# Optimization experiments

Measured on AMD Instinct MI355X. Metric: run time of the kernel, lower is better.

## Reference

```python
import jax, jax.numpy as jnp
import numpy as np

D_MODEL, D_K, D_V, D_H, SEQ = 1024, 64, 64, 16, 4096


def setup_inputs() -> dict:
    key = jax.random.key(0)
    ks = jax.random.split(key, 16)
    s = lambda fan_in: 1.0 / np.sqrt(fan_in)
    return {
        "X": jax.random.normal(ks[0], (SEQ, D_MODEL), jnp.float32),
        # shared Q/K/V projections (nn.Linear stores weight as [out, in])
        "Wq": jax.random.uniform(ks[1], (D_K, D_MODEL), jnp.float32, -s(D_MODEL), s(D_MODEL)),
        "bq": jax.random.uniform(ks[2], (D_K,), jnp.float32, -s(D_MODEL), s(D_MODEL)),
        "Wk": jax.random.uniform(ks[3], (D_K, D_MODEL), jnp.float32, -s(D_MODEL), s(D_MODEL)),
        "bk": jax.random.uniform(ks[4], (D_K,), jnp.float32, -s(D_MODEL), s(D_MODEL)),
        "Wv": jax.random.uniform(ks[5], (D_V, D_MODEL), jnp.float32, -s(D_MODEL), s(D_MODEL)),
        "bv": jax.random.uniform(ks[6], (D_V,), jnp.float32, -s(D_MODEL), s(D_MODEL)),
        # per-head linears stacked along head axis
        "Whq": jax.random.uniform(ks[7], (D_H, D_K, D_K), jnp.float32, -s(D_K), s(D_K)),
        "bhq": jax.random.uniform(ks[8], (D_H, D_K), jnp.float32, -s(D_K), s(D_K)),
        "Whk": jax.random.uniform(ks[9], (D_H, D_K, D_K), jnp.float32, -s(D_K), s(D_K)),
        "bhk": jax.random.uniform(ks[10], (D_H, D_K), jnp.float32, -s(D_K), s(D_K)),
        "Whv": jax.random.uniform(ks[11], (D_H, D_V, D_V), jnp.float32, -s(D_V), s(D_V)),
        "bhv": jax.random.uniform(ks[12], (D_H, D_V), jnp.float32, -s(D_V), s(D_V)),
        # final projection: d_h*d_v -> d_model
        "Wo": jax.random.uniform(ks[13], (D_MODEL, D_H * D_V), jnp.float32, -s(D_H * D_V), s(D_H * D_V)),
        "bo": jax.random.uniform(ks[14], (D_MODEL,), jnp.float32, -s(D_H * D_V), s(D_H * D_V)),
    }


def reference(X, Wq, bq, Wk, bk, Wv, bv, Whq, bhq, Whk, bhk, Whv, bhv, Wo, bo):
    # shared projections: [T, d_k] / [T, d_v]
    Q = X @ Wq.T + bq
    K = X @ Wk.T + bk
    V = X @ Wv.T + bv
    # per-head linears, all heads at once: [H, T, d_k]
    qh = jnp.einsum("tk,hjk->htj", Q, Whq) + bhq[:, None, :]
    kh = jnp.einsum("tk,hjk->htj", K, Whk) + bhk[:, None, :]
    vh = jnp.einsum("tv,hjv->htj", V, Whv) + bhv[:, None, :]
    # scaled dot-product attention per head: [H, T, T]
    scale = 1.0 / jnp.sqrt(jnp.asarray(Q.shape[-1], X.dtype))
    attn = jax.nn.softmax(jnp.einsum("htk,hsk->hts", qh, kh) * scale, axis=-1)
    rep = jnp.einsum("hts,hsv->htv", attn, vh)  # [H, T, d_v]
    # hstack heads -> [T, H*d_v], then final projection
    concat = rep.transpose(1, 0, 2).reshape(X.shape[0], -1)
    return concat @ Wo.T + bo
```

## Files before the change

### kernel.cpp

```cpp
#include <hip/hip_runtime.h>

#define T 4096
#define DM 1024
#define DK 64
#define H 16

typedef short s8 __attribute__((ext_vector_type(8)));
typedef float f4 __attribute__((ext_vector_type(4)));
typedef unsigned short us4 __attribute__((ext_vector_type(4)));
typedef unsigned u32x4 __attribute__((ext_vector_type(4)));
typedef __bf16 bf2 __attribute__((ext_vector_type(2)));

#define MFMA16(a,b,c) __builtin_amdgcn_mfma_f32_16x16x32_bf16((a),(b),(c),0,0,0)
#define SCALE_Q 0.18033688011112042f

__device__ __forceinline__ unsigned short f2bf(float x){
  __bf16 b = (__bf16)x;
  return __builtin_bit_cast(unsigned short, b);
}
__device__ __forceinline__ unsigned pk2(float a, float b){
  bf2 v; v[0] = (__bf16)a; v[1] = (__bf16)b;
  return __builtin_bit_cast(unsigned, v);
}

__device__ __forceinline__ void gload16(const void* g, void* lds){
  __builtin_amdgcn_global_load_lds((const __attribute__((address_space(1))) unsigned int*)g,
                                   (__attribute__((address_space(3))) unsigned int*)lds,
                                   16, 0, 0);
}

__device__ __forceinline__ void xch(unsigned X, unsigned Y, unsigned &E, unsigned &O){
#if __has_builtin(__builtin_amdgcn_permlane32_swap) && __has_builtin(__builtin_amdgcn_permlane16_swap)
  auto a = __builtin_amdgcn_permlane32_swap(X, Y, false, false);
  auto b = __builtin_amdgcn_permlane16_swap(a[0], a[1], false, false);
  E = b[0]; O = b[1];
#else
  int l = threadIdx.x & 63;
  int idxE = ((((l >> 4) & 1) * 32 + (l & 15))) << 2;
  unsigned eX = __builtin_amdgcn_ds_bpermute(idxE, X);
  unsigned eY = __builtin_amdgcn_ds_bpermute(idxE, Y);
  E = (l < 32) ? eX : eY;
  unsigned oX = __builtin_amdgcn_ds_bpermute(idxE + 64, X);
  unsigned oY = __builtin_amdgcn_ds_bpermute(idxE + 64, Y);
  O = (l < 32) ? oX : oY;
#endif
}

__global__ void cvt_bf16(const float* __restrict__ in, unsigned short* __restrict__ out, int n4){
  int i = blockIdx.x * blockDim.x + threadIdx.x;
  if (i >= n4) return;
  float4 v = reinterpret_cast<const float4*>(in)[i];
  us4 o;
  o[0] = f2bf(v.x); o[1] = f2bf(v.y); o[2] = f2bf(v.z); o[3] = f2bf(v.w);
  reinterpret_cast<us4*>(out)[i] = o;
}

#define N_WOB (DM * DM / 4)
#define N_W3  (64 * DM / 4)
#define N_WH  (16 * 64 * 64 / 4)
__global__ __launch_bounds__(256) void prep_all(
    const float* __restrict__ Wo,
    const float* __restrict__ Wq, const float* __restrict__ Wk, const float* __restrict__ Wv,
    const float* __restrict__ Whq, const float* __restrict__ Whk, const float* __restrict__ Whv,
    const float* __restrict__ bq, const float* __restrict__ bk, const float* __restrict__ bv,
    const float* __restrict__ bhq, const float* __restrict__ bhk, const float* __restrict__ bhv,
    unsigned short* __restrict__ Wob, unsigned short* __restrict__ W3b,
    unsigned short* __restrict__ Whb, float* __restrict__ beff){
  int idx = blockIdx.x * 256 + threadIdx.x;
  if (idx < N_WOB){
    float4 v = reinterpret_cast<const float4*>(Wo)[idx];
    us4 o; o[0]=f2bf(v.x); o[1]=f2bf(v.y); o[2]=f2bf(v.z); o[3]=f2bf(v.w);
    reinterpret_cast<us4*>(Wob)[idx] = o;
    return;
  }
  idx -= N_WOB;
  if (idx < 3 * N_W3){
    int seg = idx / N_W3, i = idx - seg * N_W3;
    const float* src = (seg == 0) ? Wq : ((seg == 1) ? Wk : Wv);
    float4 v = reinterpret_cast<const float4*>(src)[i];
    us4 o; o[0]=f2bf(v.x); o[1]=f2bf(v.y); o[2]=f2bf(v.z); o[3]=f2bf(v.w);
    reinterpret_cast<us4*>(W3b)[seg * N_W3 + i] = o;
    return;
  }
  idx -= 3 * N_W3;
  if (idx < 3 * N_WH){
    int seg = idx / N_WH, i = idx - seg * N_WH;
    const float* src = (seg == 0) ? Whq : ((seg == 1) ? Whk : Whv);
    float s = (seg == 0) ? SCALE_Q : 1.0f;
    float4 v = reinterpret_cast<const float4*>(src)[i];
    us4 o; o[0]=f2bf(v.x*s); o[1]=f2bf(v.y*s); o[2]=f2bf(v.z*s); o[3]=f2bf(v.w*s);
    reinterpret_cast<us4*>(Whb)[seg * N_WH + i] = o;
    return;
  }
  idx -= 3 * N_WH;
  if (idx < 3072){
    int seg = idx >> 10, j = idx & 1023;
    const float* Wh = (seg == 0) ? Whq : ((seg == 1) ? Whk : Whv);
    const float* b  = (seg == 0) ? bq  : ((seg == 1) ? bk  : bv);
    const float* bh = (seg == 0) ? bhq : ((seg == 1) ? bhk : bhv);
    float s = (seg == 0) ? SCALE_Q : 1.0f;
    const float* wr = Wh + j * 64;
    float acc = 0.f;
    #pragma unroll 8
    for (int k = 0; k < 64; ++k) acc += wr[k] * b[k];
    beff[idx] = (acc + bh[j]) * s;
  }
}

template<int MODE, int BN, int NT>
__global__ __launch_bounds__(256) void gemmX(const unsigned short* __restrict__ A,
                       const unsigned short* __restrict__ B,
                       const float* __restrict__ bias,
                       unsigned short* __restrict__ q_out,
                       unsigned short* __restrict__ k_out,
                       unsigned short* __restrict__ v_out,
                       float* __restrict__ f_out){
  __shared__ __align__(16) short la[2][128 * 64];
  __shared__ __align__(16) short lb[2][BN * 64];
  const int tid = threadIdx.x;
  const int wv = tid >> 6, l = tid & 63;
  const int lr = l & 15, lh = l >> 4;
  const int wr = wv >> 1, wc = wv & 1;
  const int tm = blockIdx.x / NT, tn = blockIdx.x % NT;
  const int t0 = tm * 128, o0 = tn * BN;
  constexpr int NF = BN / 32;
  constexpr int BCH = BN * 64 / (8 * 256);
  constexpr int LBB = BN * 128;

  f4 acc[4][NF];
  #pragma unroll
  for (int i = 0; i < 4; ++i)
    #pragma unroll
    for (int j = 0; j < NF; ++j) acc[i][j] = (f4){0.f, 0.f, 0.f, 0.f};

  const int srow = tid >> 3;
  const int scs  = (tid & 7) ^ (srow & 7);
  const unsigned short* ap = A + (size_t)(t0 + srow) * DM + scs * 8;
  const unsigned short* bp = B + (size_t)(o0 + srow) * DM + scs * 8;
  char* ad = (char*)&la[0][0] + tid * 16;
  char* bd = (char*)&lb[0][0] + tid * 16;

  auto stage = [&](int BUF){
    #pragma unroll
    for (int i = 0; i < 4; ++i)
      gload16(ap + (size_t)i * 32 * DM, ad + BUF * 16384 + i * 4096);
    #pragma unroll
    for (int i = 0; i < BCH; ++i)
      gload16(bp + (size_t)i * 32 * DM, bd + BUF * LBB + i * 4096);
    ap += 64; bp += 64;
  };

  const int asw0 = (lh ^ (lr & 7)) * 16, asw1 = ((lh ^ 4) ^ (lr & 7)) * 16;
  const char* aB0 = (const char*)&la[0][0] + (wr * 64 + lr) * 128 + asw0;
  const char* aB1 = (const char*)&la[0][0] + (wr * 64 + lr) * 128 + asw1;
  const char* bB0 = (const char*)&lb[0][0] + (wc * (BN / 2) + lr) * 128 + asw0;
  const char* bB1 = (const char*)&lb[0][0] + (wc * (BN / 2) + lr) * 128 + asw1;

  auto step = [&](int BUF, bool dostage){
    if (dostage) stage(BUF ^ 1);
    s8 af[4][2], bfr[NF][2];
    #pragma unroll
    for (int mf = 0; mf < 4; ++mf){
      af[mf][0] = *(const s8*)(aB0 + BUF * 16384 + mf * 2048);
      af[mf][1] = *(const s8*)(aB1 + BUF * 16384 + mf * 2048);
    }
    #pragma unroll
    for (int nf = 0; nf < NF; ++nf){
      bfr[nf][0] = *(const s8*)(bB0 + BUF * LBB + nf * 2048);
      bfr[nf][1] = *(const s8*)(bB1 + BUF * LBB + nf * 2048);
    }
    __builtin_amdgcn_s_setprio(1);
    #pragma unroll
    for (int mf = 0; mf < 4; ++mf)
      #pragma unroll
      for (int nf = 0; nf < NF; ++nf){
        acc[mf][nf] = MFMA16(af[mf][0], bfr[nf][0], acc[mf][nf]);
        acc[mf][nf] = MFMA16(af[mf][1], bfr[nf][1], acc[mf][nf]);
      }
    __builtin_amdgcn_s_setprio(0);
    __syncthreads();
  };

  stage(0);
  __syncthreads();
  #pragma unroll 1
  for (int t2 = 0; t2 < 8; ++t2){
    step(0, true);
    step(1, t2 < 7);
  }

  #pragma unroll
  for (int nf = 0; nf < NF; ++nf){
    int o = o0 + wc * (BN / 2) + nf * 16 + lr;
    float bs = (MODE == 4) ? 0.f : bias[o];
    int sel = o >> 6, oc = o & 63;
    unsigned short* yo = (sel == 0) ? q_out : ((sel == 1) ? k_out : v_out);
    #pragma unroll
    for (int mf = 0; mf < 4; ++mf)
      #pragma unroll
      for (int r = 0; r < 4; ++r){
        int t = t0 + wr * 64 + mf * 16 + lh * 4 + r;
        float v = acc[mf][nf][r] + bs;
        if (MODE == 2) f_out[(size_t)t * DM + o] = v;
        else           yo[(size_t)t * 64 + oc] = f2bf(v);
      }
  }
}

__global__ __launch_bounds__(256) void gemm_heads(const unsigned short* __restrict__ Yq,
                        const unsigned short* __restrict__ Yk,
                        const unsigned short* __restrict__ Yv,
                        const unsigned short* __restrict__ Whb,
                        const float* __restrict__ beff,
                        unsigned short* __restrict__ qhb,
                        unsigned short* __restrict__ khb,
                        unsigned short* __restrict__ vtb){
  const int tid = threadIdx.x;
  const int wv = tid >> 6, l = tid & 63;
  const int lr = l & 15, lh = l >> 4;
  const int rem = blockIdx.x % 48, tb = blockIdx.x / 48;
  const int kind = rem >> 4, h = rem & 15;
  const unsigned short* Y = (kind == 0) ? Yq : ((kind == 1) ? Yk : Yv);
  const unsigned short* B = Whb + (size_t)rem * 4096;
  const int t0 = tb * 256 + wv * 64;

  s8 wf[4][2], yf[4][2];
  #pragma unroll
  for (int nf = 0; nf < 4; ++nf)
    #pragma unroll
    for (int hf = 0; hf < 2; ++hf)
      wf[nf][hf] = *reinterpret_cast<const s8*>(B + (size_t)(nf * 16 + lr) * 64 + hf * 32 + lh * 8);
  #pragma unroll
  for (int mf = 0; mf < 4; ++mf)
    #pragma unroll
    for (int hf = 0; hf < 2; ++hf)
      yf[mf][hf] = *reinterpret_cast<const s8*>(Y + (size_t)(t0 + mf * 16 + lr) * 64 + hf * 32 + lh * 8);

  f4 acc[4][4];
  #pragma unroll
  for (int i = 0; i < 4; ++i)
    #pragma unroll
    for (int j = 0; j < 4; ++j) acc[i][j] = (f4){0.f, 0.f, 0.f, 0.f};

  if (kind < 2){
    #pragma unroll
    for (int mf = 0; mf < 4; ++mf)
      #pragma unroll
      for (int nf = 0; nf < 4; ++nf){
        acc[mf][nf] = MFMA16(yf[mf][0], wf[nf][0], acc[mf][nf]);
        acc[mf][nf] = MFMA16(yf[mf][1], wf[nf][1], acc[mf][nf]);
      }
    unsigned short* out = (kind == 0) ? qhb : khb;
    #pragma unroll
    for (int nf = 0; nf < 4; ++nf){
      int j = nf * 16 + lr;
      float bs = beff[rem * 64 + j];
      #pragma unroll
      for (int mf = 0; mf < 4; ++mf)
        #pragma unroll
        for (int r = 0; r < 4; ++r){
          int t = t0 + mf * 16 + lh * 4 + r;
          out[((size_t)h * T + t) * DK + j] = f2bf(acc[mf][nf][r] + bs);
        }
    }
  } else {
    #pragma unroll
    for (int nf = 0; nf < 4; ++nf)
      #pragma unroll
      for (int mf = 0; mf < 4; ++mf){
        acc[nf][mf] = MFMA16(wf[nf][0], yf[mf][0], acc[nf][mf]);
        acc[nf][mf] = MFMA16(wf[nf][1], yf[mf][1], acc[nf][mf]);
      }
    #pragma unroll
    for (int nf = 0; nf < 4; ++nf){
      float4 bsv = *reinterpret_cast<const float4*>(beff + rem * 64 + nf * 16 + lh * 4);
      #pragma unroll
      for (int r = 0; r < 4; ++r){
        int j = nf * 16 + lh * 4 + r;
        float bs = (r == 0) ? bsv.x : ((r == 1) ? bsv.y : ((r == 2) ? bsv.z : bsv.w));
        #pragma unroll
        for (int mf = 0; mf < 4; ++mf){
          int t = t0 + mf * 16 + lr;
          vtb[((size_t)h * DK + j) * T + t] = f2bf(acc[nf][mf][r] + bs);
        }
      }
    }
  }
}

__global__ __launch_bounds__(256) void attn_fwd(const unsigned short* __restrict__ qh,
                         const unsigned short* __restrict__ kh,
                         const unsigned short* __restrict__ vt,
                         unsigned short* __restrict__ cat){
  __shared__ __align__(16) short lk[2][64 * 64];
  __shared__ __align__(16) short lv[2][64 * 64];
  const int tid = threadIdx.x;
  const int wv = tid >> 6, l = tid & 63;
  const int lr = l & 15, lh = l >> 4;
  const int h = blockIdx.x >> 5, qblk = blockIdx.x & 31;
  const int Q0 = qblk * 128 + wv * 32;

  s8 qf[2][2];
  #pragma unroll
  for (int qb = 0; qb < 2; ++qb)
    #pragma unroll
    for (int hf = 0; hf < 2; ++hf)
      qf[qb][hf] = *reinterpret_cast<const s8*>(
          qh + ((size_t)h * T + Q0 + qb * 16 + lr) * DK + hf * 32 + lh * 8);

  float ls[2] = {0.f, 0.f};
  f4 oa[2][4];
  #pragma unroll
  for (int qb = 0; qb < 2; ++qb)
    #pragma unroll
    for (int jb = 0; jb < 4; ++jb) oa[qb][jb] = (f4){0.f, 0.f, 0.f, 0.f};

  const int srow = tid >> 3;
  const int scs  = (tid & 7) ^ (srow & 7);
  const unsigned short* kp = kh + (size_t)h * T * DK + srow * DK + scs * 8;
  const unsigned short* vp = vt + (size_t)h * DK * T + srow * T + scs * 8;
  char* kd = (char*)&lk[0][0] + tid * 16;
  char* vd = (char*)&lv[0][0] + tid * 16;

  auto stage = [&](int BUF){
    gload16(kp,           kd + BUF * 8192);
    gload16(kp + 32 * DK, kd + BUF * 8192 + 4096);
    gload16(vp,           vd + BUF * 8192);
    gload16(vp + 32 * T,  vd + BUF * 8192 + 4096);
    kp += 64 * DK; vp += 64;
  };

  const int sw0 = (lh ^ (lr & 7)) * 16, sw1 = ((lh ^ 4) ^ (lr & 7)) * 16;
  const char* kB0 = (const char*)&lk[0][0] + lr * 128 + sw0;
  const char* kB1 = (const char*)&lk[0][0] + lr * 128 + sw1;
  const char* vB0 = (const char*)&lv[0][0] + lr * 128 + sw0;
  const char* vB1 = (const char*)&lv[0][0] + lr * 128 + sw1;

  auto step = [&](int BUF, bool dostage){
    if (dostage) stage(BUF ^ 1);
    s8 kf[4][2], vf[4][2];
    #pragma unroll
    for (int mt = 0; mt < 4; ++mt){
      kf[mt][0] = *(const s8*)(kB0 + BUF * 8192 + mt * 2048);
      kf[mt][1] = *(const s8*)(kB1 + BUF * 8192 + mt * 2048);
      vf[mt][0] = *(const s8*)(vB0 + BUF * 8192 + mt * 2048);
      vf[mt][1] = *(const s8*)(vB1 + BUF * 8192 + mt * 2048);
    }
    #pragma unroll
    for (int qb = 0; qb < 2; ++qb){
      f4 sc[4];
      __builtin_amdgcn_s_setprio(1);
      #pragma unroll
      for (int mt = 0; mt < 4; ++mt){
        f4 z = (f4){0.f, 0.f, 0.f, 0.f};
        z = MFMA16(kf[mt][0], qf[qb][0], z);
        z = MFMA16(kf[mt][1], qf[qb][1], z);
        sc[mt] = z;
      }
      __builtin_amdgcn_s_setprio(0);
      float p[4][4];
      float rs0 = 0.f, rs1 = 0.f;
      #pragma unroll
      for (int mt = 0; mt < 4; ++mt){
        p[mt][0] = __builtin_amdgcn_exp2f(sc[mt][0]);
        p[mt][1] = __builtin_amdgcn_exp2f(sc[mt][1]);
        p[mt][2] = __builtin_amdgcn_exp2f(sc[mt][2]);
        p[mt][3] = __builtin_amdgcn_exp2f(sc[mt][3]);
        rs0 += p[mt][0] + p[mt][1];
        rs1 += p[mt][2] + p[mt][3];
      }
      ls[qb] += rs0 + rs1;
      unsigned w00 = pk2(p[0][0], p[0][1]), w01 = pk2(p[0][2], p[0][3]);
      unsigned w10 = pk2(p[1][0], p[1][1]), w11 = pk2(p[1][2], p[1][3]);
      unsigned w20 = pk2(p[2][0], p[2][1]), w21 = pk2(p[2][2], p[2][3]);
      unsigned w30 = pk2(p[3][0], p[3][1]), w31 = pk2(p[3][2], p[3][3]);
      unsigned e0, o0x, e1, o1x, e2, o2x, e3, o3x;
      xch(w00, w10, e0, o0x);
      xch(w01, w11, e1, o1x);
      xch(w20, w30, e2, o2x);
      xch(w21, w31, e3, o3x);
      u32x4 pa0u = {e0, e1, o0x, o1x};
      u32x4 pa1u = {e2, e3, o2x, o3x};
      s8 pa0 = __builtin_bit_cast(s8, pa0u);
      s8 pa1 = __builtin_bit_cast(s8, pa1u);
      __builtin_amdgcn_s_setprio(1);
      #pragma unroll
      for (int jb = 0; jb < 4; ++jb){
        oa[qb][jb] = MFMA16(pa0, vf[jb][0], oa[qb][jb]);
        oa[qb][jb] = MFMA16(pa1, vf[jb][1], oa[qb][jb]);
      }
      __builtin_amdgcn_s_setprio(0);
    }
    __syncthreads();
  };

  stage(0);
  __syncthreads();
  #pragma unroll 1
  for (int t2 = 0; t2 < 32; ++t2){
    step(0, true);
    step(1, t2 < 31);
  }

  #pragma unroll
  for (int qb = 0; qb < 2; ++qb){
    float lq = ls[qb];
    lq += __shfl_xor(lq, 16);
    lq += __shfl_xor(lq, 32);
    #pragma unroll
    for (int r = 0; r < 4; ++r){
      float lsr = __shfl(lq, lh * 4 + r);
      float inv = 1.f / lsr;
      int t = Q0 + qb * 16 + lh * 4 + r;
      #pragma unroll
      for (int jb = 0; jb < 4; ++jb)
        cat[(size_t)t * DM + h * DK + jb * 16 + lr] = f2bf(oa[qb][jb][r] * inv);
    }
  }
}

extern "C" void kernel_launch(void* const* d_in, const int* in_sizes, int n_in,
                              void* d_out, int out_size, void* d_ws, size_t ws_size,
                              hipStream_t stream){
  const float* X   = (const float*)d_in[0];
  const float* Wq  = (const float*)d_in[1];
  const float* bq  = (const float*)d_in[2];
  const float* Wk  = (const float*)d_in[3];
  const float* bk  = (const float*)d_in[4];
  const float* Wv  = (const float*)d_in[5];
  const float* bv  = (const float*)d_in[6];
  const float* Whq = (const float*)d_in[7];
  const float* bhq = (const float*)d_in[8];
  const float* Whk = (const float*)d_in[9];
  const float* bhk = (const float*)d_in[10];
  const float* Whv = (const float*)d_in[11];
  const float* bhv = (const float*)d_in[12];
  const float* Wo  = (const float*)d_in[13];
  const float* bo  = (const float*)d_in[14];

  char* w = (char*)d_ws;
  size_t off = 0;
  auto alloc = [&](size_t bytes) -> char* {
    char* p = w + off;
    off = (off + bytes + 255) & ~(size_t)255;
    return p;
  };
  unsigned short* Xbf = (unsigned short*)alloc((size_t)T * DM * 2);
  unsigned short* Wob = (unsigned short*)alloc((size_t)DM * DM * 2);
  unsigned short* W3b = (unsigned short*)alloc((size_t)192 * DM * 2);
  unsigned short* Whb = (unsigned short*)alloc((size_t)48 * 64 * 64 * 2);
  float* beff = (float*)alloc(48 * 64 * 4);
  unsigned short* Yq  = (unsigned short*)alloc((size_t)T * 64 * 2);
  unsigned short* Yk  = (unsigned short*)alloc((size_t)T * 64 * 2);
  unsigned short* Yv  = (unsigned short*)alloc((size_t)T * 64 * 2);
  unsigned short* qhb = (unsigned short*)alloc((size_t)H * T * DK * 2);
  unsigned short* khb = (unsigned short*)alloc((size_t)H * T * DK * 2);
  unsigned short* vtb = (unsigned short*)alloc((size_t)H * T * DK * 2);
  unsigned short* cat = Xbf;

  cvt_bf16<<<(T * DM / 4) / 256, 256, 0, stream>>>(X, Xbf, T * DM / 4);
  {
    int total = N_WOB + 3 * N_W3 + 3 * N_WH + 3072;
    prep_all<<<(total + 255) / 256, 256, 0, stream>>>(
        Wo, Wq, Wk, Wv, Whq, Whk, Whv, bq, bk, bv, bhq, bhk, bhv,
        Wob, W3b, Whb, beff);
  }

  gemmX<4, 64, 3><<<(T / 128) * 3, 256, 0, stream>>>(Xbf, W3b, nullptr, Yq, Yk, Yv, nullptr);

  gemm_heads<<<(T / 256) * 48, 256, 0, stream>>>(Yq, Yk, Yv, Whb, beff, qhb, khb, vtb);

  attn_fwd<<<(T / 128) * H, 256, 0, stream>>>(qhb, khb, vtb, cat);

  gemmX<2, 64, 16><<<(T / 128) * 16, 256, 0, stream>>>(cat, Wob, bo, nullptr, nullptr, nullptr, (float*)d_out);
}
```

Measured before the change: 146.7 us.

## Restructure attention into single-wave blocks with direct V loads from global

```diff
diff --git a/kernel.cpp b/kernel.cpp
--- a/kernel.cpp
+++ b/kernel.cpp
@@ -288,66 +288,78 @@
   }
 }
 
-__global__ __launch_bounds__(256) void attn_fwd(const unsigned short* __restrict__ qh,
+__global__ __launch_bounds__(64) void attn_fwd(const unsigned short* __restrict__ qh,
                          const unsigned short* __restrict__ kh,
                          const unsigned short* __restrict__ vt,
                          unsigned short* __restrict__ cat){
   __shared__ __align__(16) short lk[2][64 * 64];
-  __shared__ __align__(16) short lv[2][64 * 64];
-  const int tid = threadIdx.x;
-  const int wv = tid >> 6, l = tid & 63;
+  const int l = threadIdx.x & 63;
   const int lr = l & 15, lh = l >> 4;
-  const int h = blockIdx.x >> 5, qblk = blockIdx.x & 31;
-  const int Q0 = qblk * 128 + wv * 32;
-
-  s8 qf[2][2];
-  #pragma unroll
-  for (int qb = 0; qb < 2; ++qb)
+  const int h = blockIdx.x >> 6, qi = blockIdx.x & 63;
+  const int Q0 = qi * 64;
+
+  s8 qf[4][2];
+  #pragma unroll
+  for (int qb = 0; qb < 4; ++qb)
     #pragma unroll
     for (int hf = 0; hf < 2; ++hf)
       qf[qb][hf] = *reinterpret_cast<const s8*>(
           qh + ((size_t)h * T + Q0 + qb * 16 + lr) * DK + hf * 32 + lh * 8);
 
-  float ls[2] = {0.f, 0.f};
-  f4 oa[2][4];
-  #pragma unroll
-  for (int qb = 0; qb < 2; ++qb)
+  float ls[4] = {0.f, 0.f, 0.f, 0.f};
+  f4 oa[4][4];
+  #pragma unroll
+  for (int qb = 0; qb < 4; ++qb)
     #pragma unroll
     for (int jb = 0; jb < 4; ++jb) oa[qb][jb] = (f4){0.f, 0.f, 0.f, 0.f};
 
-  const int srow = tid >> 3;
-  const int scs  = (tid & 7) ^ (srow & 7);
+  const int srow = l >> 3;
+  const int scs  = (l & 7) ^ (srow & 7);
   const unsigned short* kp = kh + (size_t)h * T * DK + srow * DK + scs * 8;
-  const unsigned short* vp = vt + (size_t)h * DK * T + srow * T + scs * 8;
-  char* kd = (char*)&lk[0][0] + tid * 16;
-  char* vd = (char*)&lv[0][0] + tid * 16;
-
-  auto stage = [&](int BUF){
-    gload16(kp,           kd + BUF * 8192);
-    gload16(kp + 32 * DK, kd + BUF * 8192 + 4096);
-    gload16(vp,           vd + BUF * 8192);
-    gload16(vp + 32 * T,  vd + BUF * 8192 + 4096);
-    kp += 64 * DK; vp += 64;
-  };
+  char* kd = (char*)&lk[0][0] + l * 16;
+
+  const unsigned short* vp0 = vt + ((size_t)h * DK + lr) * T + lh * 8;
+  const unsigned short* vp1 = vp0 + (size_t)16 * T;
+  const unsigned short* vp2 = vp0 + (size_t)32 * T;
+  const unsigned short* vp3 = vp0 + (size_t)48 * T;
 
   const int sw0 = (lh ^ (lr & 7)) * 16, sw1 = ((lh ^ 4) ^ (lr & 7)) * 16;
   const char* kB0 = (const char*)&lk[0][0] + lr * 128 + sw0;
   const char* kB1 = (const char*)&lk[0][0] + lr * 128 + sw1;
-  const char* vB0 = (const char*)&lv[0][0] + lr * 128 + sw0;
-  const char* vB1 = (const char*)&lv[0][0] + lr * 128 + sw1;
-
-  auto step = [&](int BUF, bool dostage){
-    if (dostage) stage(BUF ^ 1);
-    s8 kf[4][2], vf[4][2];
+
+  #pragma unroll
+  for (int i = 0; i < 8; ++i) gload16(kp + i * 8 * DK, kd + i * 1024);
+  kp += 64 * DK;
+
+  #pragma unroll 1
+  for (int it = 0; it < 64; ++it){
+    const int BUF = it & 1;
+    asm volatile("s_waitcnt vmcnt(0)" ::: "memory");
+    __builtin_amdgcn_sched_barrier(0);
+
+    s8 vf[4][2];
+    vf[0][0] = *(const s8*)(vp0); vf[0][1] = *(const s8*)(vp0 + 32);
+    vf[1][0] = *(const s8*)(vp1); vf[1][1] = *(const s8*)(vp1 + 32);
+    vf[2][0] = *(const s8*)(vp2); vf[2][1] = *(const s8*)(vp2 + 32);
+    vf[3][0] = *(const s8*)(vp3); vf[3][1] = *(const s8*)(vp3 + 32);
+    vp0 += 64; vp1 += 64; vp2 += 64; vp3 += 64;
+
+    if (it < 63){
+      char* kdn = kd + (BUF ^ 1) * 8192;
+      #pragma unroll
+      for (int i = 0; i < 8; ++i) gload16(kp + i * 8 * DK, kdn + i * 1024);
+      kp += 64 * DK;
+    }
+
+    s8 kf[4][2];
     #pragma unroll
     for (int mt = 0; mt < 4; ++mt){
       kf[mt][0] = *(const s8*)(kB0 + BUF * 8192 + mt * 2048);
       kf[mt][1] = *(const s8*)(kB1 + BUF * 8192 + mt * 2048);
-      vf[mt][0] = *(const s8*)(vB0 + BUF * 8192 + mt * 2048);
-      vf[mt][1] = *(const s8*)(vB1 + BUF * 8192 + mt * 2048);
-    }
-    #pragma unroll
-    for (int qb = 0; qb < 2; ++qb){
+    }
+
+    #pragma unroll
+    for (int qb = 0; qb < 4; ++qb){
       f4 sc[4];
       __builtin_amdgcn_s_setprio(1);
       #pragma unroll
@@ -391,19 +403,10 @@
       }
       __builtin_amdgcn_s_setprio(0);
     }
-    __syncthreads();
-  };
-
-  stage(0);
-  __syncthreads();
-  #pragma unroll 1
-  for (int t2 = 0; t2 < 32; ++t2){
-    step(0, true);
-    step(1, t2 < 31);
-  }
-
-  #pragma unroll
-  for (int qb = 0; qb < 2; ++qb){
+  }
+
+  #pragma unroll
+  for (int qb = 0; qb < 4; ++qb){
     float lq = ls[qb];
     lq += __shfl_xor(lq, 16);
     lq += __shfl_xor(lq, 32);
@@ -470,7 +473,7 @@
 
   gemm_heads<<<(T / 256) * 48, 256, 0, stream>>>(Yq, Yk, Yv, Whb, beff, qhb, khb, vtb);
 
-  attn_fwd<<<(T / 128) * H, 256, 0, stream>>>(qhb, khb, vtb, cat);
+  attn_fwd<<<(T / 64) * H, 64, 0, stream>>>(qhb, khb, vtb, cat);
 
   gemmX<2, 64, 16><<<(T / 128) * 16, 256, 0, stream>>>(cat, Wob, bo, nullptr, nullptr, nullptr, (float*)d_out);
 }
```

Result: slower. 234.8 us (+60.1%).

## Split attention over two key halves with a combine kernel; shrink QKV GEMM tile

Applied to the files above, without the earlier changes.

```diff
diff --git a/kernel.cpp b/kernel.cpp
--- a/kernel.cpp
+++ b/kernel.cpp
@@ -107,7 +107,7 @@
   }
 }
 
-template<int MODE, int BN, int NT>
+template<int MODE, int BM, int BN, int NT>
 __global__ __launch_bounds__(256) void gemmX(const unsigned short* __restrict__ A,
                        const unsigned short* __restrict__ B,
                        const float* __restrict__ bias,
@@ -115,21 +115,24 @@
                        unsigned short* __restrict__ k_out,
                        unsigned short* __restrict__ v_out,
                        float* __restrict__ f_out){
-  __shared__ __align__(16) short la[2][128 * 64];
+  __shared__ __align__(16) short la[2][BM * 64];
   __shared__ __align__(16) short lb[2][BN * 64];
   const int tid = threadIdx.x;
   const int wv = tid >> 6, l = tid & 63;
   const int lr = l & 15, lh = l >> 4;
   const int wr = wv >> 1, wc = wv & 1;
   const int tm = blockIdx.x / NT, tn = blockIdx.x % NT;
-  const int t0 = tm * 128, o0 = tn * BN;
+  const int t0 = tm * BM, o0 = tn * BN;
+  constexpr int MF = BM / 32;
   constexpr int NF = BN / 32;
-  constexpr int BCH = BN * 64 / (8 * 256);
+  constexpr int ACH = BM / 32;
+  constexpr int BCH = BN / 32;
+  constexpr int LAB = BM * 128;
   constexpr int LBB = BN * 128;
 
-  f4 acc[4][NF];
-  #pragma unroll
-  for (int i = 0; i < 4; ++i)
+  f4 acc[MF][NF];
+  #pragma unroll
+  for (int i = 0; i < MF; ++i)
     #pragma unroll
     for (int j = 0; j < NF; ++j) acc[i][j] = (f4){0.f, 0.f, 0.f, 0.f};
 
@@ -142,8 +145,8 @@
 
   auto stage = [&](int BUF){
     #pragma unroll
-    for (int i = 0; i < 4; ++i)
-      gload16(ap + (size_t)i * 32 * DM, ad + BUF * 16384 + i * 4096);
+    for (int i = 0; i < ACH; ++i)
+      gload16(ap + (size_t)i * 32 * DM, ad + BUF * LAB + i * 4096);
     #pragma unroll
     for (int i = 0; i < BCH; ++i)
       gload16(bp + (size_t)i * 32 * DM, bd + BUF * LBB + i * 4096);
@@ -151,18 +154,18 @@
   };
 
   const int asw0 = (lh ^ (lr & 7)) * 16, asw1 = ((lh ^ 4) ^ (lr & 7)) * 16;
-  const char* aB0 = (const char*)&la[0][0] + (wr * 64 + lr) * 128 + asw0;
-  const char* aB1 = (const char*)&la[0][0] + (wr * 64 + lr) * 128 + asw1;
+  const char* aB0 = (const char*)&la[0][0] + (wr * (BM / 2) + lr) * 128 + asw0;
+  const char* aB1 = (const char*)&la[0][0] + (wr * (BM / 2) + lr) * 128 + asw1;
   const char* bB0 = (const char*)&lb[0][0] + (wc * (BN / 2) + lr) * 128 + asw0;
   const char* bB1 = (const char*)&lb[0][0] + (wc * (BN / 2) + lr) * 128 + asw1;
 
   auto step = [&](int BUF, bool dostage){
     if (dostage) stage(BUF ^ 1);
-    s8 af[4][2], bfr[NF][2];
-    #pragma unroll
-    for (int mf = 0; mf < 4; ++mf){
-      af[mf][0] = *(const s8*)(aB0 + BUF * 16384 + mf * 2048);
-      af[mf][1] = *(const s8*)(aB1 + BUF * 16384 + mf * 2048);
+    s8 af[MF][2], bfr[NF][2];
+    #pragma unroll
+    for (int mf = 0; mf < MF; ++mf){
+      af[mf][0] = *(const s8*)(aB0 + BUF * LAB + mf * 2048);
+      af[mf][1] = *(const s8*)(aB1 + BUF * LAB + mf * 2048);
     }
     #pragma unroll
     for (int nf = 0; nf < NF; ++nf){
@@ -171,7 +174,7 @@
     }
     __builtin_amdgcn_s_setprio(1);
     #pragma unroll
-    for (int mf = 0; mf < 4; ++mf)
+    for (int mf = 0; mf < MF; ++mf)
       #pragma unroll
       for (int nf = 0; nf < NF; ++nf){
         acc[mf][nf] = MFMA16(af[mf][0], bfr[nf][0], acc[mf][nf]);
@@ -196,10 +199,10 @@
     int sel = o >> 6, oc = o & 63;
     unsigned short* yo = (sel == 0) ? q_out : ((sel == 1) ? k_out : v_out);
     #pragma unroll
-    for (int mf = 0; mf < 4; ++mf)
+    for (int mf = 0; mf < MF; ++mf)
       #pragma unroll
       for (int r = 0; r < 4; ++r){
-        int t = t0 + wr * 64 + mf * 16 + lh * 4 + r;
+        int t = t0 + wr * (BM / 2) + mf * 16 + lh * 4 + r;
         float v = acc[mf][nf][r] + bs;
         if (MODE == 2) f_out[(size_t)t * DM + o] = v;
         else           yo[(size_t)t * 64 + oc] = f2bf(v);
@@ -288,17 +291,20 @@
   }
 }
 
-__global__ __launch_bounds__(256) void attn_fwd(const unsigned short* __restrict__ qh,
+__global__ __launch_bounds__(256, 4) void attn_fwd(const unsigned short* __restrict__ qh,
                          const unsigned short* __restrict__ kh,
                          const unsigned short* __restrict__ vt,
-                         unsigned short* __restrict__ cat){
+                         float* __restrict__ Op, float* __restrict__ lv){
   __shared__ __align__(16) short lk[2][64 * 64];
-  __shared__ __align__(16) short lv[2][64 * 64];
+  __shared__ __align__(16) short lv_[2][64 * 64];
   const int tid = threadIdx.x;
   const int wv = tid >> 6, l = tid & 63;
   const int lr = l & 15, lh = l >> 4;
-  const int h = blockIdx.x >> 5, qblk = blockIdx.x & 31;
+  const int h = blockIdx.x >> 6;
+  const int qblk = (blockIdx.x >> 1) & 31;
+  const int half = blockIdx.x & 1;
   const int Q0 = qblk * 128 + wv * 32;
+  const int S0 = half * (T / 2);
 
   s8 qf[2][2];
   #pragma unroll
@@ -317,10 +323,10 @@
 
   const int srow = tid >> 3;
   const int scs  = (tid & 7) ^ (srow & 7);
-  const unsigned short* kp = kh + (size_t)h * T * DK + srow * DK + scs * 8;
-  const unsigned short* vp = vt + (size_t)h * DK * T + srow * T + scs * 8;
+  const unsigned short* kp = kh + (size_t)h * T * DK + (size_t)S0 * DK + srow * DK + scs * 8;
+  const unsigned short* vp = vt + (size_t)h * DK * T + S0 + srow * T + scs * 8;
   char* kd = (char*)&lk[0][0] + tid * 16;
-  char* vd = (char*)&lv[0][0] + tid * 16;
+  char* vd = (char*)&lv_[0][0] + tid * 16;
 
   auto stage = [&](int BUF){
     gload16(kp,           kd + BUF * 8192);
@@ -333,8 +339,8 @@
   const int sw0 = (lh ^ (lr & 7)) * 16, sw1 = ((lh ^ 4) ^ (lr & 7)) * 16;
   const char* kB0 = (const char*)&lk[0][0] + lr * 128 + sw0;
   const char* kB1 = (const char*)&lk[0][0] + lr * 128 + sw1;
-  const char* vB0 = (const char*)&lv[0][0] + lr * 128 + sw0;
-  const char* vB1 = (const char*)&lv[0][0] + lr * 128 + sw1;
+  const char* vB0 = (const char*)&lv_[0][0] + lr * 128 + sw0;
+  const char* vB1 = (const char*)&lv_[0][0] + lr * 128 + sw1;
 
   auto step = [&](int BUF, bool dostage){
     if (dostage) stage(BUF ^ 1);
@@ -397,26 +403,46 @@
   stage(0);
   __syncthreads();
   #pragma unroll 1
-  for (int t2 = 0; t2 < 32; ++t2){
+  for (int t2 = 0; t2 < 16; ++t2){
     step(0, true);
-    step(1, t2 < 31);
-  }
-
+    step(1, t2 < 15);
+  }
+
+  const size_t base = (size_t)(half * H + h) * T;
   #pragma unroll
   for (int qb = 0; qb < 2; ++qb){
     float lq = ls[qb];
     lq += __shfl_xor(lq, 16);
     lq += __shfl_xor(lq, 32);
+    if (lh == 0) lv[base + Q0 + qb * 16 + lr] = lq;
     #pragma unroll
     for (int r = 0; r < 4; ++r){
-      float lsr = __shfl(lq, lh * 4 + r);
-      float inv = 1.f / lsr;
-      int t = Q0 + qb * 16 + lh * 4 + r;
+      size_t row = base + Q0 + qb * 16 + lh * 4 + r;
       #pragma unroll
       for (int jb = 0; jb < 4; ++jb)
-        cat[(size_t)t * DM + h * DK + jb * 16 + lr] = f2bf(oa[qb][jb][r] * inv);
-    }
-  }
+        Op[(row << 6) + jb * 16 + lr] = oa[qb][jb][r];
+    }
+  }
+}
+
+__global__ __launch_bounds__(256) void attn_combine(const float* __restrict__ Op,
+                              const float* __restrict__ lv,
+                              unsigned short* __restrict__ cat){
+  int idx = blockIdx.x * 256 + threadIdx.x;
+  int c4 = idx & 15;
+  int t = (idx >> 4) & (T - 1);
+  int h = idx >> 16;
+  size_t r0 = (size_t)h * T + t;
+  size_t r1 = (size_t)(H + h) * T + t;
+  float inv = 1.f / (lv[r0] + lv[r1]);
+  float4 a = reinterpret_cast<const float4*>(Op)[(r0 << 4) + c4];
+  float4 b = reinterpret_cast<const float4*>(Op)[(r1 << 4) + c4];
+  us4 o;
+  o[0] = f2bf((a.x + b.x) * inv);
+  o[1] = f2bf((a.y + b.y) * inv);
+  o[2] = f2bf((a.z + b.z) * inv);
+  o[3] = f2bf((a.w + b.w) * inv);
+  *reinterpret_cast<us4*>(&cat[(size_t)t * DM + h * DK + c4 * 4]) = o;
 }
 
 extern "C" void kernel_launch(void* const* d_in, const int* in_sizes, int n_in,
@@ -456,6 +482,8 @@
   unsigned short* qhb = (unsigned short*)alloc((size_t)H * T * DK * 2);
   unsigned short* khb = (unsigned short*)alloc((size_t)H * T * DK * 2);
   unsigned short* vtb = (unsigned short*)alloc((size_t)H * T * DK * 2);
+  float* Oparts = (float*)alloc((size_t)2 * H * T * DK * 4);
+  float* lvals  = (float*)alloc((size_t)2 * H * T * 4);
   unsigned short* cat = Xbf;
 
   cvt_bf16<<<(T * DM / 4) / 256, 256, 0, stream>>>(X, Xbf, T * DM / 4);
@@ -466,11 +494,12 @@
         Wob, W3b, Whb, beff);
   }
 
-  gemmX<4, 64, 3><<<(T / 128) * 3, 256, 0, stream>>>(Xbf, W3b, nullptr, Yq, Yk, Yv, nullptr);
+  gemmX<4, 64, 64, 3><<<(T / 64) * 3, 256, 0, stream>>>(Xbf, W3b, nullptr, Yq, Yk, Yv, nullptr);
 
   gemm_heads<<<(T / 256) * 48, 256, 0, stream>>>(Yq, Yk, Yv, Whb, beff, qhb, khb, vtb);
 
-  attn_fwd<<<(T / 128) * H, 256, 0, stream>>>(qhb, khb, vtb, cat);
-
-  gemmX<2, 64, 16><<<(T / 128) * 16, 256, 0, stream>>>(cat, Wob, bo, nullptr, nullptr, nullptr, (float*)d_out);
-}
+  attn_fwd<<<(T / 128) * H * 2, 256, 0, stream>>>(qhb, khb, vtb, Oparts, lvals);
+  attn_combine<<<(H * T * 16) / 256, 256, 0, stream>>>(Oparts, lvals, cat);
+
+  gemmX<2, 128, 64, 16><<<(T / 128) * 16, 256, 0, stream>>>(cat, Wob, bo, nullptr, nullptr, nullptr, (float*)d_out);
+}
```

Result: slower. 376.2 us (+156.4%).
